# Kernel tuning notes

Hardware: AMD Instinct MI355X
Metric: run time of the kernel (lower is better)

Reference implementation:

```python
import jax, jax.numpy as jnp
import numpy as np

DEFAULT_MASK_VALUE = -0.7 * float(jnp.finfo(jnp.dtype('float32')).max)

B, T, NQ, NKV, D = 2, 1024, 32, 8, 128


def setup_inputs() -> dict:
    key = jax.random.key(0)
    k1, k2, k3, k4 = jax.random.split(key, 4)
    query = jax.random.normal(k1, (B, T, NQ, D), dtype=jnp.float32)
    kk = jax.random.normal(k2, (B, T, NKV, D), dtype=jnp.float32)
    vv = jax.random.normal(k3, (B, T, NKV, D), dtype=jnp.float32)
    # packed-sequence segment ids, sorted so each segment is contiguous (values 1..3, >0 = active)
    decoder_segment_ids = jnp.sort(jax.random.randint(k4, (B, T), 1, 4), axis=-1).astype(jnp.int32)
    return {"query": query, "key": kk, "value": vv,
            "decoder_segment_ids": decoder_segment_ids}


def _attention(query, key, value, decoder_segment_ids):
    # MaxText AttentionOp.apply_attention_dot (prefill / train mode), GQA layout.
    b, t, n, d = query.shape
    n_kv = key.shape[2]
    g = n // n_kv
    q = query.reshape(b, t, n_kv, g, d)
    # qk product: [b, n_kv, g, t, s]
    logits = jnp.einsum('btkgd,bskd->bkgts', q, key)
    # generate_attention_mask: segment mask AND causal mask
    seg_mask = decoder_segment_ids[:, :, None] == decoder_segment_ids[:, None, :]  # [b,t,s]
    row_ids = jax.lax.broadcasted_iota(jnp.int32, (t, t), 0)
    col_ids = jax.lax.broadcasted_iota(jnp.int32, (t, t), 1)
    causal = col_ids <= row_ids  # [t,s]
    mask = jnp.logical_and(seg_mask, causal[None])  # [b,t,s]
    # apply_mask_to_logits: replace masked entries with DEFAULT_MASK_VALUE (avoids add fusion)
    masked = jnp.where(mask[:, None, None, :, :], logits, DEFAULT_MASK_VALUE)
    probs = jax.nn.softmax(masked, axis=-1)
    out = jnp.einsum('bkgts,bskd->btkgd', probs, value)
    return out.reshape(b, t, n, d)


def reference(query, key, value, decoder_segment_ids):
    return _attention(query, key, value, decoder_segment_ids)
```

## Files before the change

kernel.cpp:

```cpp
#include <hip/hip_runtime.h>

constexpr int B_  = 2;
constexpr int T_  = 1024;
constexpr int NQ  = 32;
constexpr int NKV = 8;
constexpr int D_  = 128;

constexpr int BM = 128;
constexpr int BN = 64;
constexpr int NTILE = T_ / BM;
constexpr float MASK_NEG = -3.0e38f;

typedef _Float16 f16;
typedef __fp16 fp16_2 __attribute__((ext_vector_type(2)));
typedef f16 f16x4 __attribute__((ext_vector_type(4)));
typedef f16 f16x8 __attribute__((ext_vector_type(8)));
typedef float floatx4 __attribute__((ext_vector_type(4)));

__device__ __align__(16) f16 g_K16 [(size_t)B_ * NKV * T_ * D_];
__device__ __align__(16) f16 g_Vt16[(size_t)B_ * NKV * T_ * D_];

__device__ __forceinline__ void dma16(const f16* g, const f16* l) {
    __builtin_amdgcn_global_load_lds(
        (const __attribute__((address_space(1))) void*)g,
        (__attribute__((address_space(3))) void*)l, 16, 0, 0);
}

__device__ __forceinline__ unsigned pk2(float a, float b) {
    union { fp16_2 h; unsigned u; } c;
    c.h = __builtin_amdgcn_cvt_pkrtz(a, b);
    return c.u;
}

__global__ __launch_bounds__(256)
void prep_kernel(const float* __restrict__ K, const float* __restrict__ V) {
    __shared__ f16 lv[64][136];
    const int sblk = blockIdx.x;
    const int kv   = blockIdx.y;
    const int b    = blockIdx.z;
    const int tid  = threadIdx.x;
    const int s0   = sblk * 64;
    const size_t inbase = ((size_t)b * T_) * NKV * D_ + (size_t)kv * D_;

    f16* kout = g_K16 + ((size_t)(b * NKV + kv) * T_ + s0) * D_;
#pragma unroll
    for (int p = 0; p < 4; ++p) {
        const int u = tid + 256 * p;
        const int s = u >> 4, ch = u & 15;
        const float* src = K + inbase + (size_t)(s0 + s) * NKV * D_ + ch * 8;
        float4 f0 = *(const float4*)src;
        float4 f1 = *(const float4*)(src + 4);
        f16x8 hh;
        hh[0] = (f16)f0.x; hh[1] = (f16)f0.y; hh[2] = (f16)f0.z; hh[3] = (f16)f0.w;
        hh[4] = (f16)f1.x; hh[5] = (f16)f1.y; hh[6] = (f16)f1.z; hh[7] = (f16)f1.w;
        *(f16x8*)(kout + s * D_ + ((ch ^ (s & 7)) * 8)) = hh;
    }
#pragma unroll
    for (int p = 0; p < 8; ++p) {
        const int u = tid + 256 * p;
        const int s = u >> 5, d4 = u & 31;
        float4 f = *(const float4*)(V + inbase + (size_t)(s0 + s) * NKV * D_ + d4 * 4);
        f16x4 hh; hh[0] = (f16)f.x; hh[1] = (f16)f.y; hh[2] = (f16)f.z; hh[3] = (f16)f.w;
        *(f16x4*)&lv[s][d4 * 4] = hh;
    }
    __syncthreads();
    f16* vout = g_Vt16 + (size_t)((b * NKV + kv) * 16 + sblk) * 8192;
#pragma unroll
    for (int p = 0; p < 4; ++p) {
        const int u = tid + 256 * p;
        const int d = u >> 3, cu = u & 7;
        f16x8 hh;
#pragma unroll
        for (int j = 0; j < 8; ++j) hh[j] = lv[cu * 8 + j][d];
        *(f16x8*)(vout + d * 64 + ((cu ^ (d & 7)) * 8)) = hh;
    }
}

#define FA_BODY(RK, RV, WK, WV, blkv)                                          \
    {                                                                          \
        const int s0 = (blkv) * BN;                                            \
        __syncthreads();                                                       \
        if ((blkv) + 1 < nblk) {                                               \
            const f16* kt = kbase + (size_t)((blkv) + 1) * 8192 + glane;       \
            const f16* vt = vbase + (size_t)((blkv) + 1) * 8192 + glane;       \
            _Pragma("unroll")                                                  \
            for (int i = 0; i < 4; ++i) {                                      \
                dma16(kt + i * 512, WK + wbase + i * 512);                     \
                dma16(vt + i * 512, WV + wbase + i * 512);                     \
            }                                                                  \
        }                                                                      \
        floatx4 sc[2][4];                                                      \
        _Pragma("unroll")                                                      \
        for (int nt = 0; nt < 4; ++nt) {                                       \
            f16x8 kf[4];                                                       \
            _Pragma("unroll")                                                  \
            for (int c = 0; c < 4; ++c)                                        \
                kf[c] = *(const f16x8*)(RK + (nt * 16 + ln) * 128 + kpc[c]);   \
            _Pragma("unroll")                                                  \
            for (int qn = 0; qn < 2; ++qn) {                                   \
                floatx4 acc = floatx4{0.f, 0.f, 0.f, 0.f};                     \
                _Pragma("unroll")                                              \
                for (int c = 0; c < 4; ++c)                                    \
                    acc = __builtin_amdgcn_mfma_f32_16x16x32_f16(kf[c], qfrag[qn][c], acc, 0, 0, 0); \
                sc[qn][nt] = acc;                                              \
            }                                                                  \
        }                                                                      \
        f16x4 pf[2][4];                                                        \
        _Pragma("unroll")                                                      \
        for (int qn = 0; qn < 2; ++qn) {                                       \
            _Pragma("unroll")                                                  \
            for (int nt = 0; nt < 4; ++nt) {                                   \
                _Pragma("unroll")                                              \
                for (int r = 0; r < 4; ++r) {                                  \
                    const int s = s0 + nt * 16 + quad * 4 + r;                 \
                    const bool ok = (s <= qrow_l[qn]) && (s >= fs_l[qn]);      \
                    sc[qn][nt][r] = ok ? sc[qn][nt][r] : MASK_NEG;             \
                }                                                              \
            }                                                                  \
            float mx = fmaxf(                                                  \
                fmaxf(fmaxf(fmaxf(sc[qn][0][0], sc[qn][0][1]), fmaxf(sc[qn][0][2], sc[qn][0][3])), \
                      fmaxf(fmaxf(sc[qn][1][0], sc[qn][1][1]), fmaxf(sc[qn][1][2], sc[qn][1][3]))), \
                fmaxf(fmaxf(fmaxf(sc[qn][2][0], sc[qn][2][1]), fmaxf(sc[qn][2][2], sc[qn][2][3])), \
                      fmaxf(fmaxf(sc[qn][3][0], sc[qn][3][1]), fmaxf(sc[qn][3][2], sc[qn][3][3])))); \
            mx = fmaxf(mx, __shfl_xor(mx, 16));                                \
            mx = fmaxf(mx, __shfl_xor(mx, 32));                                \
            const float mnew = fmaxf(m_i[qn], mx);                             \
            const float av = __expf(m_i[qn] - mnew);                           \
            m_i[qn] = mnew;                                                    \
            float ts = 0.f;                                                    \
            _Pragma("unroll")                                                  \
            for (int nt = 0; nt < 4; ++nt) {                                   \
                _Pragma("unroll")                                              \
                for (int r = 0; r < 4; ++r) {                                  \
                    sc[qn][nt][r] = __expf(sc[qn][nt][r] - mnew);              \
                    ts += sc[qn][nt][r];                                       \
                }                                                              \
            }                                                                  \
            ts += __shfl_xor(ts, 16);                                          \
            ts += __shfl_xor(ts, 32);                                          \
            l_i[qn] = l_i[qn] * av + ts;                                       \
            _Pragma("unroll")                                                  \
            for (int dt = 0; dt < 8; ++dt) o_acc[qn][dt] *= av;                \
            _Pragma("unroll")                                                  \
            for (int nt = 0; nt < 4; ++nt) {                                   \
                union { unsigned u[2]; f16x4 h; } pu;                          \
                pu.u[0] = pk2(sc[qn][nt][0], sc[qn][nt][1]);                   \
                pu.u[1] = pk2(sc[qn][nt][2], sc[qn][nt][3]);                   \
                pf[qn][nt] = pu.h;                                             \
            }                                                                  \
        }                                                                      \
        _Pragma("unroll")                                                      \
        for (int dt = 0; dt < 8; ++dt) {                                       \
            const f16* vr = RV + (dt * 16 + ln) * 64;                          \
            _Pragma("unroll")                                                  \
            for (int nt = 0; nt < 4; ++nt) {                                   \
                f16x4 va = *(const f16x4*)(vr + vpc[nt]);                      \
                o_acc[0][dt] = __builtin_amdgcn_mfma_f32_16x16x16f16(va, pf[0][nt], o_acc[0][dt], 0, 0, 0); \
                o_acc[1][dt] = __builtin_amdgcn_mfma_f32_16x16x16f16(va, pf[1][nt], o_acc[1][dt], 0, 0, 0); \
            }                                                                  \
        }                                                                      \
    }

__global__ __launch_bounds__(256, 2)
void fa_kernel(const float* __restrict__ Qg, const int* __restrict__ seg,
               float* __restrict__ Og) {
    __shared__ __align__(16) f16 kb0[64 * 128];
    __shared__ __align__(16) f16 kb1[64 * 128];
    __shared__ __align__(16) f16 vb0[128 * 64];
    __shared__ __align__(16) f16 vb1[128 * 64];
    __shared__ int lds_seg[T_];

    const int xt   = (int)((blockIdx.x + blockIdx.y) & 7);
    const int tile = blockIdx.z ? (7 - xt) : xt;
    const int h    = blockIdx.y;
    const int b    = blockIdx.z;
    const int kv   = h >> 2;

    const int tid  = threadIdx.x;
    const int wave = tid >> 6;
    const int lane = tid & 63;
    const int quad = lane >> 4;
    const int ln   = lane & 15;
    const int sw   = ln & 7;

    int kpc[4];
#pragma unroll
    for (int c = 0; c < 4; ++c) kpc[c] = ((4 * c + quad) ^ sw) * 8;
    int vpc[4];
#pragma unroll
    for (int nt = 0; nt < 4; ++nt)
        vpc[nt] = (((2 * nt + (quad >> 1)) ^ sw) * 8) + (quad & 1) * 4;

    const int glane = wave * 2048 + lane * 8;
    const int wbase = wave * 2048;

    const f16* kbase = g_K16 + (size_t)(b * NKV + kv) * T_ * D_;
    const f16* vbase = g_Vt16 + (size_t)(b * NKV + kv) * T_ * D_;

    *(int4*)&lds_seg[tid * 4] = *(const int4*)(seg + b * T_ + tid * 4);

    const int t0 = tile * BM;

    int qrow_l[2];
    f16x8 qfrag[2][4];
#pragma unroll
    for (int qn = 0; qn < 2; ++qn) {
        qrow_l[qn] = t0 + wave * 32 + qn * 16 + ln;
        const float* qptr = Qg + (((size_t)b * T_ + qrow_l[qn]) * NQ + h) * D_;
#pragma unroll
        for (int c = 0; c < 4; ++c) {
            const float* p = qptr + c * 32 + quad * 8;
            float4 f0 = *(const float4*)(p);
            float4 f1 = *(const float4*)(p + 4);
            f16x8 v;
            v[0] = (f16)f0.x; v[1] = (f16)f0.y; v[2] = (f16)f0.z; v[3] = (f16)f0.w;
            v[4] = (f16)f1.x; v[5] = (f16)f1.y; v[6] = (f16)f1.z; v[7] = (f16)f1.w;
            qfrag[qn][c] = v;
        }
    }

    __syncthreads();

    int fs_l[2];
#pragma unroll
    for (int qn = 0; qn < 2; ++qn) {
        const int segq = lds_seg[qrow_l[qn]];
        int lo = 0, hi = qrow_l[qn];
        while (lo < hi) {
            const int mid = (lo + hi) >> 1;
            if (lds_seg[mid] < segq) lo = mid + 1; else hi = mid;
        }
        fs_l[qn] = lo;
    }

    const int seg_lo = lds_seg[t0];
    unsigned long long bal = __ballot(lds_seg[lane * 16 + 15] < seg_lo);
    const int blk_start = __popcll(bal) >> 2;
    const int nblk = 2 * (tile + 1);

    float  m_i[2] = { -1.0e30f, -1.0e30f };
    float  l_i[2] = { 0.f, 0.f };
    floatx4 o_acc[2][8];
#pragma unroll
    for (int qn = 0; qn < 2; ++qn)
#pragma unroll
        for (int dt = 0; dt < 8; ++dt) o_acc[qn][dt] = floatx4{0.f, 0.f, 0.f, 0.f};

    {
        const f16* kt = kbase + (size_t)blk_start * 8192 + glane;
        const f16* vt = vbase + (size_t)blk_start * 8192 + glane;
#pragma unroll
        for (int i = 0; i < 4; ++i) {
            dma16(kt + i * 512, kb0 + wbase + i * 512);
            dma16(vt + i * 512, vb0 + wbase + i * 512);
        }
    }

    int blk = blk_start;
    while (true) {
        FA_BODY(kb0, vb0, kb1, vb1, blk)
        if (++blk >= nblk) break;
        FA_BODY(kb1, vb1, kb0, vb0, blk)
        if (++blk >= nblk) break;
    }

#pragma unroll
    for (int qn = 0; qn < 2; ++qn) {
        const float inv = 1.0f / l_i[qn];
        float* optr = Og + (((size_t)b * T_ + qrow_l[qn]) * NQ + h) * D_;
#pragma unroll
        for (int dt = 0; dt < 8; ++dt) {
            floatx4 o = o_acc[qn][dt];
            o[0] *= inv; o[1] *= inv; o[2] *= inv; o[3] *= inv;
            *(floatx4*)(optr + dt * 16 + quad * 4) = o;
        }
    }
}

extern "C" void kernel_launch(void* const* d_in, const int* in_sizes, int n_in,
                              void* d_out, int out_size, void* d_ws, size_t ws_size,
                              hipStream_t stream) {
    const float* Q   = (const float*)d_in[0];
    const float* K   = (const float*)d_in[1];
    const float* V   = (const float*)d_in[2];
    const int*   seg = (const int*)d_in[3];
    float* out = (float*)d_out;

    dim3 pgrid(16, NKV, B_);
    prep_kernel<<<pgrid, 256, 0, stream>>>(K, V);

    dim3 grid(NTILE, NQ, B_);
    fa_kernel<<<grid, 256, 0, stream>>>(Q, seg, out);
}
```

Before: 121.1 us.

## Split KV blocks across two wave groups per block and merge softmax partials

```diff
diff --git a/kernel.cpp b/kernel.cpp
--- a/kernel.cpp
+++ b/kernel.cpp
@@ -7,8 +7,6 @@
 constexpr int D_  = 128;
 
 constexpr int BM = 128;
-constexpr int BN = 64;
-constexpr int NTILE = T_ / BM;
 constexpr float MASK_NEG = -3.0e38f;
 
 typedef _Float16 f16;
@@ -64,34 +62,38 @@
         *(f16x4*)&lv[s][d4 * 4] = hh;
     }
     __syncthreads();
-    f16* vout = g_Vt16 + (size_t)((b * NKV + kv) * 16 + sblk) * 8192;
+    f16* vout = g_Vt16 + (size_t)((b * NKV + kv) * 32 + sblk * 2) * 4096;
 #pragma unroll
     for (int p = 0; p < 4; ++p) {
         const int u = tid + 256 * p;
-        const int d = u >> 3, cu = u & 7;
+        const int hb = u >> 9, rem = u & 511;
+        const int d = rem >> 2, ch = rem & 3;
         f16x8 hh;
 #pragma unroll
-        for (int j = 0; j < 8; ++j) hh[j] = lv[cu * 8 + j][d];
-        *(f16x8*)(vout + d * 64 + ((cu ^ (d & 7)) * 8)) = hh;
-    }
-}
-
-#define FA_BODY(RK, RV, WK, WV, blkv)                                          \
+        for (int j = 0; j < 8; ++j) hh[j] = lv[hb * 32 + ch * 8 + j][d];
+        *(f16x8*)(vout + hb * 4096 + d * 32 + ((ch ^ (d & 3)) << 3)) = hh;
+    }
+}
+
+#define SB(DB, scur)                                                           \
     {                                                                          \
-        const int s0 = (blkv) * BN;                                            \
         __syncthreads();                                                       \
-        if ((blkv) + 1 < nblk) {                                               \
-            const f16* kt = kbase + (size_t)((blkv) + 1) * 8192 + glane;       \
-            const f16* vt = vbase + (size_t)((blkv) + 1) * 8192 + glane;       \
-            _Pragma("unroll")                                                  \
-            for (int i = 0; i < 4; ++i) {                                      \
-                dma16(kt + i * 512, WK + wbase + i * 512);                     \
-                dma16(vt + i * 512, WV + wbase + i * 512);                     \
-            }                                                                  \
+        if ((scur) + 1 < send) {                                               \
+            const int bb = 2 * ((scur) + 1) + g;                               \
+            const f16* kt = kbase + (size_t)bb * 4096 + stg;                   \
+            const f16* vt = vbase + (size_t)bb * 4096 + stg;                   \
+            const int o = ((DB) ^ 1) * 16384;                                  \
+            dma16(kt,       smem + o + myK0 + stw);                            \
+            dma16(kt + 512, smem + o + myK0 + stw + 512);                      \
+            dma16(vt,       smem + o + myV0 + stw);                            \
+            dma16(vt + 512, smem + o + myV0 + stw + 512);                      \
         }                                                                      \
-        floatx4 sc[2][4];                                                      \
+        const f16* RK = smem + (DB) * 16384 + myK0;                            \
+        const f16* RV = smem + (DB) * 16384 + myV0;                            \
+        const int skey0 = (scur) * 64 + g * 32;                                \
+        floatx4 sc[2][2];                                                      \
         _Pragma("unroll")                                                      \
-        for (int nt = 0; nt < 4; ++nt) {                                       \
+        for (int nt = 0; nt < 2; ++nt) {                                       \
             f16x8 kf[4];                                                       \
             _Pragma("unroll")                                                  \
             for (int c = 0; c < 4; ++c)                                        \
@@ -105,23 +107,21 @@
                 sc[qn][nt] = acc;                                              \
             }                                                                  \
         }                                                                      \
-        f16x4 pf[2][4];                                                        \
+        f16x4 pf[2][2];                                                        \
         _Pragma("unroll")                                                      \
         for (int qn = 0; qn < 2; ++qn) {                                       \
             _Pragma("unroll")                                                  \
-            for (int nt = 0; nt < 4; ++nt) {                                   \
+            for (int nt = 0; nt < 2; ++nt) {                                   \
                 _Pragma("unroll")                                              \
                 for (int r = 0; r < 4; ++r) {                                  \
-                    const int s = s0 + nt * 16 + quad * 4 + r;                 \
+                    const int s = skey0 + nt * 16 + quad * 4 + r;              \
                     const bool ok = (s <= qrow_l[qn]) && (s >= fs_l[qn]);      \
                     sc[qn][nt][r] = ok ? sc[qn][nt][r] : MASK_NEG;             \
                 }                                                              \
             }                                                                  \
             float mx = fmaxf(                                                  \
-                fmaxf(fmaxf(fmaxf(sc[qn][0][0], sc[qn][0][1]), fmaxf(sc[qn][0][2], sc[qn][0][3])), \
-                      fmaxf(fmaxf(sc[qn][1][0], sc[qn][1][1]), fmaxf(sc[qn][1][2], sc[qn][1][3]))), \
-                fmaxf(fmaxf(fmaxf(sc[qn][2][0], sc[qn][2][1]), fmaxf(sc[qn][2][2], sc[qn][2][3])), \
-                      fmaxf(fmaxf(sc[qn][3][0], sc[qn][3][1]), fmaxf(sc[qn][3][2], sc[qn][3][3])))); \
+                fmaxf(fmaxf(sc[qn][0][0], sc[qn][0][1]), fmaxf(sc[qn][0][2], sc[qn][0][3])), \
+                fmaxf(fmaxf(sc[qn][1][0], sc[qn][1][1]), fmaxf(sc[qn][1][2], sc[qn][1][3]))); \
             mx = fmaxf(mx, __shfl_xor(mx, 16));                                \
             mx = fmaxf(mx, __shfl_xor(mx, 32));                                \
             const float mnew = fmaxf(m_i[qn], mx);                             \
@@ -129,7 +129,7 @@
             m_i[qn] = mnew;                                                    \
             float ts = 0.f;                                                    \
             _Pragma("unroll")                                                  \
-            for (int nt = 0; nt < 4; ++nt) {                                   \
+            for (int nt = 0; nt < 2; ++nt) {                                   \
                 _Pragma("unroll")                                              \
                 for (int r = 0; r < 4; ++r) {                                  \
                     sc[qn][nt][r] = __expf(sc[qn][nt][r] - mnew);              \
@@ -142,7 +142,7 @@
             _Pragma("unroll")                                                  \
             for (int dt = 0; dt < 8; ++dt) o_acc[qn][dt] *= av;                \
             _Pragma("unroll")                                                  \
-            for (int nt = 0; nt < 4; ++nt) {                                   \
+            for (int nt = 0; nt < 2; ++nt) {                                   \
                 union { unsigned u[2]; f16x4 h; } pu;                          \
                 pu.u[0] = pk2(sc[qn][nt][0], sc[qn][nt][1]);                   \
                 pu.u[1] = pk2(sc[qn][nt][2], sc[qn][nt][3]);                   \
@@ -151,9 +151,9 @@
         }                                                                      \
         _Pragma("unroll")                                                      \
         for (int dt = 0; dt < 8; ++dt) {                                       \
-            const f16* vr = RV + (dt * 16 + ln) * 64;                          \
-            _Pragma("unroll")                                                  \
-            for (int nt = 0; nt < 4; ++nt) {                                   \
+            const f16* vr = RV + (dt * 16 + ln) * 32;                          \
+            _Pragma("unroll")                                                  \
+            for (int nt = 0; nt < 2; ++nt) {                                   \
                 f16x4 va = *(const f16x4*)(vr + vpc[nt]);                      \
                 o_acc[0][dt] = __builtin_amdgcn_mfma_f32_16x16x16f16(va, pf[0][nt], o_acc[0][dt], 0, 0, 0); \
                 o_acc[1][dt] = __builtin_amdgcn_mfma_f32_16x16x16f16(va, pf[1][nt], o_acc[1][dt], 0, 0, 0); \
@@ -161,23 +161,22 @@
         }                                                                      \
     }
 
-__global__ __launch_bounds__(256, 2)
+__global__ __launch_bounds__(512, 4)
 void fa_kernel(const float* __restrict__ Qg, const int* __restrict__ seg,
                float* __restrict__ Og) {
-    __shared__ __align__(16) f16 kb0[64 * 128];
-    __shared__ __align__(16) f16 kb1[64 * 128];
-    __shared__ __align__(16) f16 vb0[128 * 64];
-    __shared__ __align__(16) f16 vb1[128 * 64];
+    __shared__ __align__(16) f16 smem[32768];
     __shared__ int lds_seg[T_];
 
-    const int xt   = (int)((blockIdx.x + blockIdx.y) & 7);
-    const int tile = blockIdx.z ? (7 - xt) : xt;
-    const int h    = blockIdx.y;
-    const int b    = blockIdx.z;
-    const int kv   = h >> 2;
+    const int x = blockIdx.x, y = blockIdx.y, b = blockIdx.z;
+    const int u = (x + (y >> 1)) & 7;
+    const int tile = (y & 1) ? (7 - u) : u;
+    const int h  = y;
+    const int kv = h >> 2;
 
     const int tid  = threadIdx.x;
     const int wave = tid >> 6;
+    const int g    = wave >> 2;
+    const int wv   = wave & 3;
     const int lane = tid & 63;
     const int quad = lane >> 4;
     const int ln   = lane & 15;
@@ -186,18 +185,20 @@
     int kpc[4];
 #pragma unroll
     for (int c = 0; c < 4; ++c) kpc[c] = ((4 * c + quad) ^ sw) * 8;
-    int vpc[4];
-#pragma unroll
-    for (int nt = 0; nt < 4; ++nt)
-        vpc[nt] = (((2 * nt + (quad >> 1)) ^ sw) * 8) + (quad & 1) * 4;
-
-    const int glane = wave * 2048 + lane * 8;
-    const int wbase = wave * 2048;
+    int vpc[2];
+#pragma unroll
+    for (int nt = 0; nt < 2; ++nt)
+        vpc[nt] = (((2 * nt + (quad >> 1)) ^ (ln & 3)) << 3) + (quad & 1) * 4;
+
+    const int myK0 = g * 4096;
+    const int myV0 = 8192 + g * 4096;
+    const int stg  = wv * 1024 + lane * 8;
+    const int stw  = wv * 1024;
 
     const f16* kbase = g_K16 + (size_t)(b * NKV + kv) * T_ * D_;
     const f16* vbase = g_Vt16 + (size_t)(b * NKV + kv) * T_ * D_;
 
-    *(int4*)&lds_seg[tid * 4] = *(const int4*)(seg + b * T_ + tid * 4);
+    *(int2*)&lds_seg[tid * 2] = *(const int2*)(seg + b * T_ + tid * 2);
 
     const int t0 = tile * BM;
 
@@ -205,7 +206,7 @@
     f16x8 qfrag[2][4];
 #pragma unroll
     for (int qn = 0; qn < 2; ++qn) {
-        qrow_l[qn] = t0 + wave * 32 + qn * 16 + ln;
+        qrow_l[qn] = t0 + wv * 32 + qn * 16 + ln;
         const float* qptr = Qg + (((size_t)b * T_ + qrow_l[qn]) * NQ + h) * D_;
 #pragma unroll
         for (int c = 0; c < 4; ++c) {
@@ -235,8 +236,8 @@
 
     const int seg_lo = lds_seg[t0];
     unsigned long long bal = __ballot(lds_seg[lane * 16 + 15] < seg_lo);
-    const int blk_start = __popcll(bal) >> 2;
-    const int nblk = 2 * (tile + 1);
+    const int s0 = __popcll(bal) >> 2;
+    const int send = 2 * (tile + 1);
 
     float  m_i[2] = { -1.0e30f, -1.0e30f };
     float  l_i[2] = { 0.f, 0.f };
@@ -247,32 +248,59 @@
         for (int dt = 0; dt < 8; ++dt) o_acc[qn][dt] = floatx4{0.f, 0.f, 0.f, 0.f};
 
     {
-        const f16* kt = kbase + (size_t)blk_start * 8192 + glane;
-        const f16* vt = vbase + (size_t)blk_start * 8192 + glane;
-#pragma unroll
-        for (int i = 0; i < 4; ++i) {
-            dma16(kt + i * 512, kb0 + wbase + i * 512);
-            dma16(vt + i * 512, vb0 + wbase + i * 512);
-        }
-    }
-
-    int blk = blk_start;
+        const int bb = 2 * s0 + g;
+        const f16* kt = kbase + (size_t)bb * 4096 + stg;
+        const f16* vt = vbase + (size_t)bb * 4096 + stg;
+        dma16(kt,       smem + myK0 + stw);
+        dma16(kt + 512, smem + myK0 + stw + 512);
+        dma16(vt,       smem + myV0 + stw);
+        dma16(vt + 512, smem + myV0 + stw + 512);
+    }
+
+    int s = s0;
     while (true) {
-        FA_BODY(kb0, vb0, kb1, vb1, blk)
-        if (++blk >= nblk) break;
-        FA_BODY(kb1, vb1, kb0, vb0, blk)
-        if (++blk >= nblk) break;
-    }
-
-#pragma unroll
-    for (int qn = 0; qn < 2; ++qn) {
-        const float inv = 1.0f / l_i[qn];
-        float* optr = Og + (((size_t)b * T_ + qrow_l[qn]) * NQ + h) * D_;
-#pragma unroll
-        for (int dt = 0; dt < 8; ++dt) {
-            floatx4 o = o_acc[qn][dt];
-            o[0] *= inv; o[1] *= inv; o[2] *= inv; o[3] *= inv;
-            *(floatx4*)(optr + dt * 16 + quad * 4) = o;
+        SB(0, s)
+        if (++s >= send) break;
+        SB(1, s)
+        if (++s >= send) break;
+    }
+
+    __syncthreads();
+    float* mlp = (float*)lds_seg;
+    float* op  = (float*)smem;
+    const int bidx = wv * 64 + lane;
+    if (g == 1) {
+        floatx4 ml;
+        ml[0] = m_i[0]; ml[1] = l_i[0]; ml[2] = m_i[1]; ml[3] = l_i[1];
+        *(floatx4*)&mlp[bidx * 4] = ml;
+#pragma unroll
+        for (int qn = 0; qn < 2; ++qn)
+#pragma unroll
+            for (int dt = 0; dt < 8; ++dt)
+                *(floatx4*)&op[bidx * 64 + qn * 32 + ((dt ^ (bidx & 7)) << 2)] = o_acc[qn][dt];
+    }
+    __syncthreads();
+    if (g == 0) {
+        const floatx4 ml = *(const floatx4*)&mlp[bidx * 4];
+#pragma unroll
+        for (int qn = 0; qn < 2; ++qn) {
+            const float mB = ml[qn * 2], lB = ml[qn * 2 + 1];
+            const float ms = fmaxf(m_i[qn], mB);
+            const float sA = __expf(m_i[qn] - ms);
+            const float sB = __expf(mB - ms);
+            const float linv = 1.0f / (l_i[qn] * sA + lB * sB);
+            const float fA = sA * linv, fB = sB * linv;
+            float* optr = Og + (((size_t)b * T_ + qrow_l[qn]) * NQ + h) * D_;
+#pragma unroll
+            for (int dt = 0; dt < 8; ++dt) {
+                floatx4 ob = *(const floatx4*)&op[bidx * 64 + qn * 32 + ((dt ^ (bidx & 7)) << 2)];
+                floatx4 o = o_acc[qn][dt];
+                o[0] = o[0] * fA + ob[0] * fB;
+                o[1] = o[1] * fA + ob[1] * fB;
+                o[2] = o[2] * fA + ob[2] * fB;
+                o[3] = o[3] * fA + ob[3] * fB;
+                *(floatx4*)(optr + dt * 16 + quad * 4) = o;
+            }
         }
     }
 }
@@ -289,6 +317,6 @@
     dim3 pgrid(16, NKV, B_);
     prep_kernel<<<pgrid, 256, 0, stream>>>(K, V);
 
-    dim3 grid(NTILE, NQ, B_);
-    fa_kernel<<<grid, 256, 0, stream>>>(Q, seg, out);
-}
+    dim3 grid(T_ / BM, NQ, B_);
+    fa_kernel<<<grid, 512, 0, stream>>>(Q, seg, out);
+}
```

Result: slower. 185.6 us (+53.2%).
